# Kernel optimization log

Measured on AMD Instinct MI355X. Metric: run time of the kernel, lower is better.

## Reference

```python
import jax, jax.numpy as jnp
import numpy as np

HEADS = 4
EPS_LN = 1e-6
EPS_IN = 1e-5


def _ln(x, g, b):
    m = x.mean(-1, keepdims=True)
    v = ((x - m) ** 2).mean(-1, keepdims=True)
    return (x - m) / jnp.sqrt(v + EPS_LN) * g + b


def _inorm(s):
    # nn.InstanceNorm2d(1) (affine=False): normalize each (batch, channel=head)
    # slice over the last two (N, N) dims, biased variance, eps=1e-5.
    m = s.mean((-2, -1), keepdims=True)
    v = ((s - m) ** 2).mean((-2, -1), keepdims=True)
    return (s - m) / jnp.sqrt(v + EPS_IN)


def setup_inputs() -> dict:
    key = jax.random.key(0)
    ks = jax.random.split(key, 32)
    B, C, Hh = 8, 256, HEADS
    sc = 1.0 / np.sqrt(C)

    def n(k, shape, s):
        return jax.random.normal(k, shape, jnp.float32) * s

    return {
        "x": n(ks[0], (B, C, 6, 6, 6), 1.0),
        # global branch params
        "g_tok_w": n(ks[1], (C,), 0.05), "g_tok_b": jnp.zeros((C,), jnp.float32),
        "g_ln1_g": jnp.ones((C,), jnp.float32), "g_ln1_b": jnp.zeros((C,), jnp.float32),
        "g_wq": n(ks[2], (C, C * Hh), sc), "g_wk": n(ks[3], (C, C * Hh), sc),
        "g_wv": n(ks[4], (C, C * Hh), sc), "g_wo": n(ks[5], (C * Hh, C), sc),
        "g_ln2_g": jnp.ones((C,), jnp.float32), "g_ln2_b": jnp.zeros((C,), jnp.float32),
        "g_mo_w": n(ks[6], (C, C), sc), "g_mo_b": jnp.zeros((C,), jnp.float32),
        # local branch params
        "l_pw": n(ks[7], (8, 8), 0.35), "l_pb": jnp.zeros((8,), jnp.float32),
        "l_ln1_g": jnp.ones((C,), jnp.float32), "l_ln1_b": jnp.zeros((C,), jnp.float32),
        "l_wq": n(ks[8], (C, C * Hh), sc), "l_wk": n(ks[9], (C, C * Hh), sc),
        "l_wv": n(ks[10], (C, C * Hh), sc), "l_wo": n(ks[11], (C * Hh, C), sc),
        "l_ln2_g": jnp.ones((C,), jnp.float32), "l_ln2_b": jnp.zeros((C,), jnp.float32),
        "l_mo_w": n(ks[12], (C, C), sc), "l_mo_b": jnp.zeros((C,), jnp.float32),
    }


def _global_branch(x, tok_w, tok_b, ln1_g, ln1_b, wq, wk, wv, wo, ln2_g, ln2_b, mo_w, mo_b):
    B, C, D, H, W = x.shape
    Hh = HEADS
    # TokenLearner_Global: conv1x1x1 (1->256) then mean over (D,H,W), then
    # view(B,C,C).mean(dim=1).  Since the conv is 1x1 on a single input channel,
    # this collapses exactly to: w * mean(x over C,D,H,W) + b.
    m = x.mean((1, 2, 3, 4))                       # (B,)
    tok = m[:, None] * tok_w + tok_b               # (B, C)
    res = tok
    t = _ln(tok, ln1_g, ln1_b)                     # (B, C)
    q = (t @ wq).reshape(B, Hh, C)                 # heads outer in the 1024 split
    k = (t @ wk).reshape(B, Hh, C)
    v = (t @ wv).reshape(B, Hh, C)
    # mh_q^T (B,h,C,1) @ mh_k (B,h,1,C) -> rank-1 (B,h,C,C) score map
    score = q[:, :, :, None] * k[:, :, None, :]
    a = jax.nn.softmax(_inorm(score), axis=-1)
    o = jnp.einsum('bhij,bhj->bhi', a, v)          # attn @ mh_v^T -> (B,h,C)
    # permute(0,3,2,1).view: flatten as (c, heads) with c outer
    o = o.transpose(0, 2, 1).reshape(B, C * Hh)
    out = o @ wo                                   # (B, C)
    tok2 = _ln(out + res, ln2_g, ln2_b)            # (B, C)
    # map_out conv1x1 + GELU on a spatially-constant expand -> compute once
    g = jax.nn.gelu(jnp.einsum('bc,oc->bo', tok2, mo_w) + mo_b, approximate=False)
    return jnp.broadcast_to(g[:, :, None, None, None], (B, C, D, H, W))


def _local_branch(x, pw, pb, ln1_g, ln1_b, wq, wk, wv, wo, ln2_g, ln2_b, mo_w, mo_b):
    B, C, D, H, W = x.shape
    Hh = HEADS
    # TokenLearner_Local: conv3d(1->8, k=2, s=2) per channel == patchify 2x2x2
    xp = x.reshape(B * C, 3, 2, 3, 2, 3, 2).transpose(0, 1, 3, 5, 2, 4, 6)
    xp = xp.reshape(B * C, 27, 8)                  # (BC, patches, patch_vol)
    tok = xp @ pw.T + pb                           # (BC, 27, 8) embed_dim=8
    tok = tok.reshape(B, C, 3, 3, 3, 2, 2, 2)
    # res: (b c)(d h w)(p1 p2 p3) -> b (d p1 h p2 w p3) c
    res = tok.transpose(0, 2, 5, 3, 6, 4, 7, 1).reshape(B, 216, C)
    # attn input: (b c)(d h w)(p1 p2 p3) -> (b d h w) (p1 p2 p3) c
    e = tok.reshape(B, C, 3, 3, 3, 8).transpose(0, 2, 3, 4, 5, 1).reshape(B * 27, 8, C)
    e = _ln(e, ln1_g, ln1_b)
    # (c heads) split: c outer, heads inner
    q = (e @ wq).reshape(B * 27, 8, C, Hh).transpose(0, 3, 2, 1)   # (B27,h,C,8)
    k = (e @ wk).reshape(B * 27, 8, C, Hh).transpose(0, 3, 1, 2)   # (B27,h,8,C)
    v = (e @ wv).reshape(B * 27, 8, C, Hh).transpose(0, 3, 2, 1)   # (B27,h,C,8)
    score = q @ k                                                  # (B27,h,C,C)
    a = jax.nn.softmax(_inorm(score), axis=-1)
    o = a @ v                                                      # (B27,h,C,8)
    # (b d h w) heads c (p1 p2 p3) -> b (d p1 h p2 w p3) (c heads)
    o = o.reshape(B, 3, 3, 3, Hh, C, 2, 2, 2)
    o = o.transpose(0, 1, 6, 2, 7, 3, 8, 5, 4).reshape(B, 216, C * Hh)
    out = o @ wo                                                   # (B,216,C)
    t2 = _ln(out + res, ln2_g, ln2_b)
    xm = t2.transpose(0, 2, 1).reshape(B, C, D, H, W)
    return jax.nn.gelu(
        jnp.einsum('bcdhw,oc->bodhw', xm, mo_w) + mo_b[None, :, None, None, None],
        approximate=False)


def reference(x,
              g_tok_w, g_tok_b, g_ln1_g, g_ln1_b, g_wq, g_wk, g_wv, g_wo,
              g_ln2_g, g_ln2_b, g_mo_w, g_mo_b,
              l_pw, l_pb, l_ln1_g, l_ln1_b, l_wq, l_wk, l_wv, l_wo,
              l_ln2_g, l_ln2_b, l_mo_w, l_mo_b):
    g = _global_branch(x, g_tok_w, g_tok_b, g_ln1_g, g_ln1_b, g_wq, g_wk, g_wv,
                       g_wo, g_ln2_g, g_ln2_b, g_mo_w, g_mo_b)
    l = _local_branch(x, l_pw, l_pb, l_ln1_g, l_ln1_b, l_wq, l_wk, l_wv,
                      l_wo, l_ln2_g, l_ln2_b, l_mo_w, l_mo_b)
    return x + g + l
```

## Files before the change

kernel.cpp:

```cpp
#include <hip/hip_runtime.h>
#include <stdint.h>
#include <math.h>

#define DEVFN __device__ __forceinline__
typedef unsigned short u16;
typedef short bf16x8 __attribute__((ext_vector_type(8)));
typedef float f32x4  __attribute__((ext_vector_type(4)));

DEVFN float blk_sum(float v, float* s4) {
  #pragma unroll
  for (int o = 32; o > 0; o >>= 1) v += __shfl_down(v, o, 64);
  __syncthreads();
  if ((threadIdx.x & 63) == 0) s4[threadIdx.x >> 6] = v;
  __syncthreads();
  return s4[0] + s4[1] + s4[2] + s4[3];
}

DEVFN float gelu_f(float x) {
  return 0.5f * x * (1.f + erff(x * 0.7071067811865475f));
}

DEVFN u16 bf16_rne(float f) {
  uint32_t u = __float_as_uint(f);
  return (u16)((u + 0x7fffu + ((u >> 16) & 1u)) >> 16);
}

DEVFN float bf2f(u16 v) { return __uint_as_float(((uint32_t)v) << 16); }

DEVFN void gload16(const u16* g, u16* l) {
  auto gp = (const __attribute__((address_space(1))) uint32_t*)(uintptr_t)g;
  auto lp = (__attribute__((address_space(3))) uint32_t*)(uintptr_t)l;
  __builtin_amdgcn_global_load_lds(gp, lp, 16, 0, 0);
}

DEVFN void stage64x256(const u16* G, size_t gstride, u16* L, int w, int lane) {
  #pragma unroll
  for (int i = 0; i < 8; ++i) {
    int row = w * 16 + 2 * i + (lane >> 5);
    int c16 = (lane & 31) ^ (row & 7);
    gload16(G + (size_t)row * gstride + c16 * 8, L + (w * 16 + 2 * i) * 256);
  }
}

DEVFN bf16x8 lread(const u16* L, int row, int k16) {
  return *(const bf16x8*)&L[row * 256 + ((k16 ^ (row & 7)) << 3)];
}

DEVFN void trc_tile(const float* __restrict__ in, u16* __restrict__ out,
                    int R, int C, int r0, int c0, float (*tile)[33], int tid) {
  int tx = tid & 31, ty = tid >> 5;
  for (int i = ty; i < 32; i += 8) tile[i][tx] = in[(size_t)(r0 + i) * C + c0 + tx];
  __syncthreads();
  for (int i = ty; i < 32; i += 8)
    out[(size_t)(c0 + i) * R + r0 + tx] = bf16_rne(tile[tx][i]);
}

__global__ __launch_bounds__(256) void k_l_tok_prep(
    const float* __restrict__ x, const float* __restrict__ pw,
    const float* __restrict__ pb, const float* __restrict__ g1,
    const float* __restrict__ b1, float* __restrict__ res,
    u16* __restrict__ eln_bf, float* __restrict__ g_part,
    const float* __restrict__ wq, const float* __restrict__ wk,
    const float* __restrict__ wv, const float* __restrict__ wo,
    const float* __restrict__ mow, u16* __restrict__ WcatT,
    u16* __restrict__ woT, u16* __restrict__ moB) {
  __shared__ __align__(16) char smem[8448];
  int bid0 = blockIdx.x, tid = threadIdx.x;
  if (bid0 < 1728) {
    float* pws = (float*)smem;
    float* s4 = (float*)(smem + 256);
    int t = bid0;
    int b = t / 216, s = t % 216;
    int z = s / 36, y = (s / 6) % 6, xx = s % 6;
    int d = z >> 1, p1 = z & 1, hh = y >> 1, p2 = y & 1, ww = xx >> 1, p3 = xx & 1;
    int p = p1 * 4 + p2 * 2 + p3;
    int c = tid;
    if (c < 64) pws[c] = pw[c];
    __syncthreads();
    const float* xb = x + (b * 256 + c) * 216 + (2 * d) * 36 + (2 * hh) * 6 + 2 * ww;
    float v = pb[p];
    float xs = 0.f;
    #pragma unroll
    for (int q1 = 0; q1 < 2; ++q1)
      #pragma unroll
      for (int q2 = 0; q2 < 2; ++q2)
        #pragma unroll
        for (int q3 = 0; q3 < 2; ++q3) {
          float xv = xb[q1 * 36 + q2 * 6 + q3];
          xs += xv;
          v += xv * pws[p * 8 + (q1 * 4 + q2 * 2 + q3)];
        }
    float bs = blk_sum(xs, s4);
    if (c == 0) g_part[t] = bs;
    res[t * 256 + c] = v;
    float mu = blk_sum(v, s4) * (1.f / 256.f);
    float dd = v - mu;
    float var = blk_sum(dd * dd, s4) * (1.f / 256.f);
    eln_bf[t * 256 + c] = bf16_rne(dd * rsqrtf(var + 1e-6f) * g1[c] + b1[c]);
  } else {
    float (*tile)[33] = (float(*)[33])smem;
    int bid = bid0 - 1728;
    if (bid < 768) {
      int which = bid >> 8, b2 = bid & 255;
      const float* in = (which == 0) ? wq : (which == 1) ? wk : wv;
      u16* out = WcatT + which * 262144;
      int r0 = (b2 & 7) * 32, c0 = (b2 >> 3) * 32;
      trc_tile(in, out, 256, 1024, r0, c0, tile, tid);
    } else if (bid < 1024) {
      int b2 = bid - 768;
      int r0 = (b2 & 31) * 32, c0 = (b2 >> 5) * 32;
      trc_tile(wo, woT, 1024, 256, r0, c0, tile, tid);
    } else {
      int i = (bid - 1024) * 256 + tid;
      moB[i] = bf16_rne(mow[i]);
    }
  }
}

__global__ __launch_bounds__(256) void k_gemm_qkv_fused(
    const u16* __restrict__ A, const u16* __restrict__ BT, u16* __restrict__ C,
    const float* __restrict__ g_part, const float* __restrict__ tw_,
    const float* __restrict__ tb_, const float* __restrict__ g1,
    const float* __restrict__ b1, const float* __restrict__ wq,
    const float* __restrict__ wk, const float* __restrict__ wv,
    float* __restrict__ gqkv) {
  __shared__ __align__(16) char smem[65536];
  int bid = blockIdx.x, tid = threadIdx.x;
  if (bid < 1296) {
    const int N = 3072, K = 256;
    u16* aL = (u16*)smem;
    u16* bL = (u16*)smem + 16384;
    int rowblk = (bid % 27) * 64, colblk = (bid / 27) * 64;
    int lane = tid & 63, w = tid >> 6;
    int wr = (w >> 1) * 32, wc = (w & 1) * 32;
    int fm = lane & 15, lg = lane >> 4;
    stage64x256(A + (size_t)rowblk * K, K, aL, w, lane);
    stage64x256(BT + (size_t)colblk * K, K, bL, w, lane);
    __syncthreads();
    f32x4 acc[2][2] = {};
    #pragma unroll
    for (int kk = 0; kk < 8; ++kk) {
      int k16 = kk * 4 + lg;
      bf16x8 bn0 = lread(bL, wc + fm, k16);
      bf16x8 bn1 = lread(bL, wc + 16 + fm, k16);
      bf16x8 af0 = lread(aL, wr + fm, k16);
      bf16x8 af1 = lread(aL, wr + 16 + fm, k16);
      acc[0][0] = __builtin_amdgcn_mfma_f32_16x16x32_bf16(af0, bn0, acc[0][0], 0, 0, 0);
      acc[0][1] = __builtin_amdgcn_mfma_f32_16x16x32_bf16(af0, bn1, acc[0][1], 0, 0, 0);
      acc[1][0] = __builtin_amdgcn_mfma_f32_16x16x32_bf16(af1, bn0, acc[1][0], 0, 0, 0);
      acc[1][1] = __builtin_amdgcn_mfma_f32_16x16x32_bf16(af1, bn1, acc[1][1], 0, 0, 0);
    }
    __syncthreads();
    u16* ct = (u16*)smem;
    #pragma unroll
    for (int mi = 0; mi < 2; ++mi)
      #pragma unroll
      for (int ni = 0; ni < 2; ++ni)
        #pragma unroll
        for (int r = 0; r < 4; ++r)
          ct[(wr + mi * 16 + lg * 4 + r) * 64 + wc + ni * 16 + fm] = bf16_rne(acc[mi][ni][r]);
    __syncthreads();
    #pragma unroll
    for (int pass = 0; pass < 2; ++pass) {
      int id = pass * 256 + tid;
      int r = id >> 3, u = id & 7;
      *(uint4*)&C[(size_t)(rowblk + r) * N + colblk + u * 8] = *(uint4*)&ct[r * 64 + u * 8];
    }
  } else {
    float* ts = (float*)smem;
    float (*red)[4][8] = (float(*)[4][8])(smem + 8192);
    float* s4 = (float*)(smem + 16384);
    float* m_s = (float*)(smem + 16400);
    int rb = bid - 1296;
    float tw = tw_[tid], tb = tb_[tid], gg = g1[tid], bb = b1[tid];
    float S1 = blk_sum(tw, s4);
    float S2 = blk_sum(tw * tw, s4);
    float S3 = blk_sum(tb, s4);
    float S4 = blk_sum(tb * tb, s4);
    float S5 = blk_sum(tw * tb, s4);
    {
      int b = tid >> 5, sl = tid & 31;
      float a = 0.f;
      for (int k = sl; k < 216; k += 32) a += g_part[b * 216 + k];
      #pragma unroll
      for (int o = 16; o > 0; o >>= 1) a += __shfl_down(a, o, 32);
      if (sl == 0) m_s[b] = a * (1.f / 442368.f);
    }
    __syncthreads();
    #pragma unroll
    for (int b = 0; b < 8; ++b) {
      float m = m_s[b];
      float mu = (m * S1 + S3) * (1.f / 256.f);
      float var = (m * m * S2 + 2.f * m * S5 + S4) * (1.f / 256.f) - mu * mu;
      ts[b * 256 + tid] = (m * tw + tb - mu) * rsqrtf(var + 1e-6f) * gg + bb;
    }
    __syncthreads();
    int col0 = rb * 64;
    int cl = tid & 63, kq = tid >> 6;
    int col = col0 + cl;
    int m = col >> 10, cc = col & 1023;
    const float* W = (m == 0) ? wq : (m == 1) ? wk : wv;
    float acc[8] = {};
    for (int c = kq * 64; c < kq * 64 + 64; ++c) {
      float w = W[c * 1024 + cc];
      #pragma unroll
      for (int b = 0; b < 8; ++b) acc[b] = fmaf(ts[b * 256 + c], w, acc[b]);
    }
    #pragma unroll
    for (int b = 0; b < 8; ++b) red[cl][kq][b] = acc[b];
    __syncthreads();
    if (kq == 0) {
      #pragma unroll
      for (int b = 0; b < 8; ++b)
        gqkv[b * 3072 + col] = red[cl][0][b] + red[cl][1][b] + red[cl][2][b] + red[cl][3][b];
    }
  }
}

__global__ __launch_bounds__(256) void k_l_attn_fused(
    const u16* __restrict__ qkv, u16* __restrict__ o_buf,
    const float* __restrict__ gq, float* __restrict__ g_o) {
  __shared__ __align__(16) uint4 Qb[256], Kb[256];
  __shared__ __align__(16) u16 vt[16][264];
  __shared__ __align__(16) u16 Pl[256][72];
  __shared__ float rqA[64][4], rkA[64][4], rlq[64][4], rlk[64][4], s_ab[2];
  int bid = blockIdx.x, tid = threadIdx.x;
  if (bid >= 864) {
    float* ks = (float*)Qb;
    float* vs = ks + 256;
    float* s4 = (float*)Kb;
    int idx = bid - 864;
    int b = idx >> 2, h = idx & 3;
    int i = tid;
    const float* base = gq + b * 3072 + h * 256;
    float q = base[i];
    float k = base[1024 + i];
    ks[i] = k;
    vs[i] = base[2048 + i];
    float sq  = blk_sum(q, s4);
    float sq2 = blk_sum(q * q, s4);
    float sk  = blk_sum(k, s4);
    float sk2 = blk_sum(k * k, s4);
    float tot  = sq * sk * (1.f / 65536.f);
    float tot2 = sq2 * sk2 * (1.f / 65536.f);
    float rstd = rsqrtf(tot2 - tot * tot + 1e-5f);
    float A = rstd, B = -tot * rstd;
    float den = 0.f, num = 0.f;
    for (int j = 0; j < 256; ++j) {
      float w = __expf(fmaf(q * ks[j], A, B));
      den += w; num += w * vs[j];
    }
    g_o[b * 1024 + (i << 2) + h] = num / den;
    return;
  }
  int n = bid >> 2, h = bid & 3;
  int b = n / 27, patch = n % 27;
  int bz = 2 * (patch / 9), by = 2 * ((patch / 3) % 3), bx = 2 * (patch % 3);
  int tid2 = tid;
  {
    int c = tid2;
    u16 qv[8], kv[8], vv[8];
    #pragma unroll
    for (int p = 0; p < 8; ++p) {
      int t_l = b * 216 + (bz + (p >> 2)) * 36 + (by + ((p >> 1) & 1)) * 6 + (bx + (p & 1));
      const u16* row = qkv + (size_t)t_l * 3072 + (c << 2) + h;
      qv[p] = row[0]; kv[p] = row[1024]; vv[p] = row[2048];
    }
    uint32_t qw[4], kw[4];
    #pragma unroll
    for (int i = 0; i < 4; ++i) {
      qw[i] = (uint32_t)qv[2 * i] | ((uint32_t)qv[2 * i + 1] << 16);
      kw[i] = (uint32_t)kv[2 * i] | ((uint32_t)kv[2 * i + 1] << 16);
    }
    Qb[c] = make_uint4(qw[0], qw[1], qw[2], qw[3]);
    Kb[c] = make_uint4(kw[0], kw[1], kw[2], kw[3]);
    #pragma unroll
    for (int p = 0; p < 8; ++p) vt[p][c] = vv[p];
    vt[8][c] = 0x3F80u;
    #pragma unroll
    for (int r2 = 9; r2 < 16; ++r2) vt[r2][c] = 0;
  }
  __syncthreads();
  {
    int p = tid2 & 63, chunk = tid2 >> 6;
    int d = p >> 3, e = p & 7;
    float aq = 0.f, ak = 0.f, lq = 0.f, lk = 0.f;
    for (int cc = chunk * 64; cc < chunk * 64 + 64; ++cc) {
      const u16* qr = (const u16*)&Qb[cc];
      const u16* kr = (const u16*)&Kb[cc];
      float qd = bf2f(qr[d]), qe = bf2f(qr[e]);
      float kd = bf2f(kr[d]), ke = bf2f(kr[e]);
      aq = fmaf(qd, qe, aq); ak = fmaf(kd, ke, ak);
      if (e == 0) { lq += qd; lk += kd; }
    }
    rqA[p][chunk] = aq; rkA[p][chunk] = ak; rlq[p][chunk] = lq; rlk[p][chunk] = lk;
    __syncthreads();
    if (tid2 < 64) {
      float gq2 = rqA[tid2][0] + rqA[tid2][1] + rqA[tid2][2] + rqA[tid2][3];
      float gk = rkA[tid2][0] + rkA[tid2][1] + rkA[tid2][2] + rkA[tid2][3];
      float vprod = gq2 * gk, vmu = 0.f;
      if ((tid2 & 7) == 0) {
        float slq = rlq[tid2][0] + rlq[tid2][1] + rlq[tid2][2] + rlq[tid2][3];
        float slk = rlk[tid2][0] + rlk[tid2][1] + rlk[tid2][2] + rlk[tid2][3];
        vmu = slq * slk;
      }
      #pragma unroll
      for (int o = 32; o > 0; o >>= 1) {
        vprod += __shfl_down(vprod, o, 64);
        vmu   += __shfl_down(vmu, o, 64);
      }
      if (tid2 == 0) {
        float mu = vmu * (1.f / 65536.f), m2 = vprod * (1.f / 65536.f);
        float rstd = rsqrtf(m2 - mu * mu + 1e-5f);
        s_ab[0] = rstd; s_ab[1] = -mu * rstd;
      }
    }
    __syncthreads();
  }
  float Af = s_ab[0], Bf = s_ab[1];
  int lane = tid2 & 63, w = tid2 >> 6;
  int l15 = lane & 15, lg = lane >> 4;
  bf16x8 qf[4];
  #pragma unroll
  for (int qt = 0; qt < 4; ++qt)
    qf[qt] = *(const bf16x8*)&Qb[w * 64 + qt * 16 + l15];
  f32x4 acc_o[4] = {};
  #pragma unroll 1
  for (int jc = 0; jc < 4; ++jc) {
    bf16x8 kf[4];
    #pragma unroll
    for (int jt = 0; jt < 4; ++jt) {
      bf16x8 z = {};
      if (lg == 0) z = *(const bf16x8*)&Kb[jc * 64 + jt * 16 + l15];
      kf[jt] = z;
    }
    #pragma unroll
    for (int jt = 0; jt < 4; ++jt) {
      #pragma unroll
      for (int qt = 0; qt < 4; ++qt) {
        f32x4 zc = {};
        f32x4 s = __builtin_amdgcn_mfma_f32_16x16x32_bf16(kf[jt], qf[qt], zc, 0, 0, 0);
        float e0 = __expf(fmaf(s[0], Af, Bf));
        float e1 = __expf(fmaf(s[1], Af, Bf));
        float e2 = __expf(fmaf(s[2], Af, Bf));
        float e3 = __expf(fmaf(s[3], Af, Bf));
        uint32_t w0 = (__float_as_uint(e0) >> 16) | (__float_as_uint(e1) & 0xFFFF0000u);
        uint32_t w1 = (__float_as_uint(e2) >> 16) | (__float_as_uint(e3) & 0xFFFF0000u);
        int q = w * 64 + qt * 16 + l15;
        *(uint2*)&Pl[q][jt * 16 + lg * 4] = make_uint2(w0, w1);
      }
    }
    #pragma unroll
    for (int ks2 = 0; ks2 < 2; ++ks2) {
      bf16x8 vf = *(const bf16x8*)&vt[l15][jc * 64 + ks2 * 32 + lg * 8];
      #pragma unroll
      for (int qt = 0; qt < 4; ++qt) {
        bf16x8 pf = *(const bf16x8*)&Pl[w * 64 + qt * 16 + l15][ks2 * 32 + lg * 8];
        acc_o[qt] = __builtin_amdgcn_mfma_f32_16x16x32_bf16(pf, vf, acc_o[qt], 0, 0, 0);
      }
    }
  }
  int src = ((lane & 48) + 8) << 2;
  int p = l15;
  int t_l = b * 216 + (bz + (p >> 2)) * 36 + (by + ((p >> 1) & 1)) * 6 + (bx + (p & 1));
  #pragma unroll
  for (int qt = 0; qt < 4; ++qt) {
    #pragma unroll
    for (int r = 0; r < 4; ++r) {
      float den = __int_as_float(__builtin_amdgcn_ds_bpermute(src, __float_as_int(acc_o[qt][r])));
      if (p < 8) {
        int q = w * 64 + qt * 16 + lg * 4 + r;
        o_buf[(size_t)t_l * 1024 + (q << 2) + h] = bf16_rne(acc_o[qt][r] / den);
      }
    }
  }
}

__global__ __launch_bounds__(256) void k_gemm_sk_fused(
    const u16* __restrict__ A, const u16* __restrict__ BT, float* __restrict__ Cp,
    const float* __restrict__ g_o, const float* __restrict__ wo,
    float* __restrict__ part) {
  __shared__ __align__(16) char smem[65536];
  int bid = blockIdx.x, tid = threadIdx.x;
  if (bid < 216) {
    const int M = 1728, N = 256, K = 1024;
    u16* aL = (u16*)smem;
    u16* bL = (u16*)smem + 16384;
    int rowblk = (bid % 27) * 64, colblk = ((bid / 27) & 3) * 64;
    int kz = bid / 108;
    float* C = Cp + (size_t)kz * M * N;
    int lane = tid & 63, w = tid >> 6;
    int wr = (w >> 1) * 32, wc = (w & 1) * 32;
    int fm = lane & 15, lg = lane >> 4;
    f32x4 acc[2][2] = {};
    #pragma unroll 1
    for (int step = 0; step < 2; ++step) {
      int kt = kz * 512 + step * 256;
      __syncthreads();
      stage64x256(A + (size_t)rowblk * K + kt, K, aL, w, lane);
      stage64x256(BT + (size_t)colblk * K + kt, K, bL, w, lane);
      __syncthreads();
      #pragma unroll
      for (int kk = 0; kk < 8; ++kk) {
        int k16 = kk * 4 + lg;
        bf16x8 bn0 = lread(bL, wc + fm, k16);
        bf16x8 bn1 = lread(bL, wc + 16 + fm, k16);
        bf16x8 af0 = lread(aL, wr + fm, k16);
        bf16x8 af1 = lread(aL, wr + 16 + fm, k16);
        acc[0][0] = __builtin_amdgcn_mfma_f32_16x16x32_bf16(af0, bn0, acc[0][0], 0, 0, 0);
        acc[0][1] = __builtin_amdgcn_mfma_f32_16x16x32_bf16(af0, bn1, acc[0][1], 0, 0, 0);
        acc[1][0] = __builtin_amdgcn_mfma_f32_16x16x32_bf16(af1, bn0, acc[1][0], 0, 0, 0);
        acc[1][1] = __builtin_amdgcn_mfma_f32_16x16x32_bf16(af1, bn1, acc[1][1], 0, 0, 0);
      }
    }
    __syncthreads();
    float* ct = (float*)smem;
    #pragma unroll
    for (int mi = 0; mi < 2; ++mi)
      #pragma unroll
      for (int ni = 0; ni < 2; ++ni)
        #pragma unroll
        for (int r = 0; r < 4; ++r)
          ct[(wr + mi * 16 + lg * 4 + r) * 64 + wc + ni * 16 + fm] = acc[mi][ni][r];
    __syncthreads();
    #pragma unroll
    for (int pass = 0; pass < 4; ++pass) {
      int id = pass * 256 + tid;
      int r = id >> 4, u = id & 15;
      *(float4*)&C[(size_t)(rowblk + r) * N + colblk + u * 4] = *(float4*)&ct[r * 64 + u * 4];
    }
  } else {
    float* os = (float*)smem;
    int kc = bid - 216;
    os[tid] = g_o[(tid >> 5) * 1024 + kc * 32 + (tid & 31)];
    __syncthreads();
    float acc[8] = {};
    #pragma unroll
    for (int kk = 0; kk < 32; ++kk) {
      float w = wo[(size_t)(kc * 32 + kk) * 256 + tid];
      #pragma unroll
      for (int b = 0; b < 8; ++b) acc[b] = fmaf(os[b * 32 + kk], w, acc[b]);
    }
    #pragma unroll
    for (int b = 0; b < 8; ++b) part[kc * 2048 + b * 256 + tid] = acc[b];
  }
}

__global__ __launch_bounds__(256) void k_l_ln2_fused(
    const float* __restrict__ proj0, const float* __restrict__ proj1,
    const float* __restrict__ res, const float* __restrict__ g2,
    const float* __restrict__ b2, u16* __restrict__ t2b,
    const float* __restrict__ part, const float* __restrict__ g_part,
    const float* __restrict__ tw_, const float* __restrict__ tb_,
    const float* __restrict__ gg2, const float* __restrict__ gb2,
    float* __restrict__ t2g) {
  __shared__ float s4[4];
  int bid = blockIdx.x, c = threadIdx.x;
  if (bid < 1728) {
    int t = bid;
    float v = proj0[t * 256 + c] + proj1[t * 256 + c] + res[t * 256 + c];
    float mu = blk_sum(v, s4) * (1.f / 256.f);
    float d = v - mu;
    float var = blk_sum(d * d, s4) * (1.f / 256.f);
    t2b[t * 256 + c] = bf16_rne(d * rsqrtf(var + 1e-6f) * g2[c] + b2[c]);
  } else {
    int b = bid - 1728;
    float a = (c < 216) ? g_part[b * 216 + c] : 0.f;
    float m = blk_sum(a, s4) * (1.f / 442368.f);
    float v = m * tw_[c] + tb_[c];
    #pragma unroll
    for (int kc = 0; kc < 32; ++kc) v += part[kc * 2048 + b * 256 + c];
    float mu = blk_sum(v, s4) * (1.f / 256.f);
    float d = v - mu;
    float var = blk_sum(d * d, s4) * (1.f / 256.f);
    t2g[b * 256 + c] = d * rsqrtf(var + 1e-6f) * gg2[c] + gb2[c];
  }
}

__global__ __launch_bounds__(256) void k_g_mo(
    const float* __restrict__ t2g, const float* __restrict__ mow,
    const float* __restrict__ mob, float* __restrict__ g_vec) {
  __shared__ float ts[2048];
  int tid = threadIdx.x;
  for (int i = tid; i < 2048; i += 256) ts[i] = t2g[i];
  __syncthreads();
  int ol = tid >> 5, cs = tid & 31;
  int o = blockIdx.x * 8 + ol;
  const float* wrow = mow + (size_t)o * 256;
  float acc[8] = {};
  #pragma unroll
  for (int i = 0; i < 8; ++i) {
    float w = wrow[i * 32 + cs];
    #pragma unroll
    for (int b = 0; b < 8; ++b) acc[b] = fmaf(ts[b * 256 + i * 32 + cs], w, acc[b]);
  }
  #pragma unroll
  for (int b = 0; b < 8; ++b) {
    float v = acc[b];
    #pragma unroll
    for (int off = 16; off > 0; off >>= 1) v += __shfl_down(v, off, 32);
    if (cs == 0) g_vec[b * 256 + o] = gelu_f(v + mob[o]);
  }
}

__global__ __launch_bounds__(256) void k_gemm_mo_final(
    const u16* __restrict__ A, const u16* __restrict__ BT,
    const float* __restrict__ x, const float* __restrict__ gvec,
    const float* __restrict__ mob, float* __restrict__ out) {
  __shared__ __align__(16) char smem[65536];
  u16* aL = (u16*)smem;
  u16* bL = (u16*)smem + 16384;
  float (*ct)[65] = (float(*)[65])smem;
  const int K = 256;
  int tid = threadIdx.x;
  int rowblk = blockIdx.x * 64, colblk = blockIdx.y * 64;
  int lane = tid & 63, w = tid >> 6;
  int wr = (w >> 1) * 32, wc = (w & 1) * 32;
  int fm = lane & 15, lg = lane >> 4;
  stage64x256(A + (size_t)rowblk * K, K, aL, w, lane);
  stage64x256(BT + (size_t)colblk * K, K, bL, w, lane);
  __syncthreads();
  f32x4 acc[2][2] = {};
  #pragma unroll
  for (int kk = 0; kk < 8; ++kk) {
    int k16 = kk * 4 + lg;
    bf16x8 bn0 = lread(bL, wc + fm, k16);
    bf16x8 bn1 = lread(bL, wc + 16 + fm, k16);
    bf16x8 af0 = lread(aL, wr + fm, k16);
    bf16x8 af1 = lread(aL, wr + 16 + fm, k16);
    acc[0][0] = __builtin_amdgcn_mfma_f32_16x16x32_bf16(af0, bn0, acc[0][0], 0, 0, 0);
    acc[0][1] = __builtin_amdgcn_mfma_f32_16x16x32_bf16(af0, bn1, acc[0][1], 0, 0, 0);
    acc[1][0] = __builtin_amdgcn_mfma_f32_16x16x32_bf16(af1, bn0, acc[1][0], 0, 0, 0);
    acc[1][1] = __builtin_amdgcn_mfma_f32_16x16x32_bf16(af1, bn1, acc[1][1], 0, 0, 0);
  }
  __syncthreads();
  int row_l0 = wr + lg * 4;
  #pragma unroll
  for (int mi = 0; mi < 2; ++mi)
    #pragma unroll
    for (int ni = 0; ni < 2; ++ni)
      #pragma unroll
      for (int r = 0; r < 4; ++r)
        ct[row_l0 + mi * 16 + r][wc + ni * 16 + fm] = acc[mi][ni][r];
  __syncthreads();
  int s_l = tid & 63;
  #pragma unroll 4
  for (int pass = 0; pass < 16; ++pass) {
    int col_l = (tid >> 6) * 16 + pass;
    int row = rowblk + s_l, col = colblk + col_l;
    int b = row / 216, s = row - b * 216;
    size_t idx = (size_t)b * 55296 + (size_t)col * 216 + s;
    out[idx] = x[idx] + gvec[b * 256 + col] + gelu_f(ct[s_l][col_l] + mob[col]);
  }
}

extern "C" void kernel_launch(void* const* d_in, const int* in_sizes, int n_in,
                              void* d_out, int out_size, void* d_ws, size_t ws_size,
                              hipStream_t stream) {
  const float* x     = (const float*)d_in[0];
  const float* g_tw  = (const float*)d_in[1];
  const float* g_tb  = (const float*)d_in[2];
  const float* g_l1g = (const float*)d_in[3];
  const float* g_l1b = (const float*)d_in[4];
  const float* g_wq  = (const float*)d_in[5];
  const float* g_wk  = (const float*)d_in[6];
  const float* g_wv  = (const float*)d_in[7];
  const float* g_wo  = (const float*)d_in[8];
  const float* g_l2g = (const float*)d_in[9];
  const float* g_l2b = (const float*)d_in[10];
  const float* g_mow = (const float*)d_in[11];
  const float* g_mob = (const float*)d_in[12];
  const float* l_pw  = (const float*)d_in[13];
  const float* l_pb  = (const float*)d_in[14];
  const float* l_l1g = (const float*)d_in[15];
  const float* l_l1b = (const float*)d_in[16];
  const float* l_wq  = (const float*)d_in[17];
  const float* l_wk  = (const float*)d_in[18];
  const float* l_wv  = (const float*)d_in[19];
  const float* l_wo  = (const float*)d_in[20];
  const float* l_l2g = (const float*)d_in[21];
  const float* l_l2b = (const float*)d_in[22];
  const float* l_mow = (const float*)d_in[23];
  const float* l_mob = (const float*)d_in[24];
  float* out = (float*)d_out;
  float* ws  = (float*)d_ws;

  float* g_qkv  = ws + 4096;
  float* g_o    = ws + 28672;
  float* g_vec  = ws + 36864;
  float* g_part = ws + 38912;
  float* res    = ws + 40960;
  u16*   eln_bf = (u16*)(ws + 483328);
  u16*   WcatT  = (u16*)(ws + 704512);
  u16*   woT    = (u16*)(ws + 1097728);
  u16*   moB    = (u16*)(ws + 1228800);
  u16*   qkvb   = (u16*)(ws + 1261568);
  u16*   o_buf  = (u16*)(ws + 6569984);
  float* proj   = ws + 7454720;
  u16*   t2b    = (u16*)(ws + 8339456);
  float* part_wo= ws + 8560640;
  float* t2g    = ws + 8626176;

  k_l_tok_prep<<<3008, 256, 0, stream>>>(x, l_pw, l_pb, l_l1g, l_l1b,
                                         res, eln_bf, g_part,
                                         l_wq, l_wk, l_wv, l_wo, l_mow,
                                         WcatT, woT, moB);
  k_gemm_qkv_fused<<<1344, 256, 0, stream>>>(eln_bf, WcatT, qkvb,
                                             g_part, g_tw, g_tb, g_l1g, g_l1b,
                                             g_wq, g_wk, g_wv, g_qkv);
  k_l_attn_fused<<<896, 256, 0, stream>>>(qkvb, o_buf, g_qkv, g_o);
  k_gemm_sk_fused<<<248, 256, 0, stream>>>(o_buf, woT, proj, g_o, g_wo, part_wo);
  k_l_ln2_fused<<<1736, 256, 0, stream>>>(proj, proj + 442368, res,
                                          l_l2g, l_l2b, t2b,
                                          part_wo, g_part, g_tw, g_tb,
                                          g_l2g, g_l2b, t2g);
  k_g_mo<<<32, 256, 0, stream>>>(t2g, g_mow, g_mob, g_vec);
  k_gemm_mo_final<<<dim3(27, 4), 256, 0, stream>>>(t2b, moB, x, g_vec, l_mob, out);
}
```

Baseline: 99.78 us.

## Split QKV GEMM from global branch, remap tiles, fuse LayerNorm reductions

Moves the global-branch QKV projection out of the fused GEMM launch into its own small kernel, so the local GEMM no longer reserves 64 KB of generic shared memory. The GEMM now stages tiles in a k-major LDS layout without XOR swizzle, remaps block indices to group tiles, and pads the output staging stride to 72. LayerNorm statistics are computed with single-pass sum and sum-of-squares reductions, which cuts the number of block barriers. The single-pass variance is less numerically robust, and the extra launch adds a serial kernel boundary.

```diff
diff --git a/kernel.cpp b/kernel.cpp
--- a/kernel.cpp
+++ b/kernel.cpp
@@ -16,6 +16,40 @@
   return s4[0] + s4[1] + s4[2] + s4[3];
 }
 
+DEVFN void blk_sum3(float a, float b, float c, float* out, float (*s)[4]) {
+  #pragma unroll
+  for (int o = 32; o > 0; o >>= 1) {
+    a += __shfl_down(a, o, 64);
+    b += __shfl_down(b, o, 64);
+    c += __shfl_down(c, o, 64);
+  }
+  __syncthreads();
+  if ((threadIdx.x & 63) == 0) {
+    int wi = threadIdx.x >> 6;
+    s[0][wi] = a; s[1][wi] = b; s[2][wi] = c;
+  }
+  __syncthreads();
+  out[0] = s[0][0] + s[0][1] + s[0][2] + s[0][3];
+  out[1] = s[1][0] + s[1][1] + s[1][2] + s[1][3];
+  out[2] = s[2][0] + s[2][1] + s[2][2] + s[2][3];
+}
+
+DEVFN void blk_sum2(float a, float b, float* out, float (*s)[4]) {
+  #pragma unroll
+  for (int o = 32; o > 0; o >>= 1) {
+    a += __shfl_down(a, o, 64);
+    b += __shfl_down(b, o, 64);
+  }
+  __syncthreads();
+  if ((threadIdx.x & 63) == 0) {
+    int wi = threadIdx.x >> 6;
+    s[0][wi] = a; s[1][wi] = b;
+  }
+  __syncthreads();
+  out[0] = s[0][0] + s[0][1] + s[0][2] + s[0][3];
+  out[1] = s[1][0] + s[1][1] + s[1][2] + s[1][3];
+}
+
 DEVFN float gelu_f(float x) {
   return 0.5f * x * (1.f + erff(x * 0.7071067811865475f));
 }
@@ -41,7 +75,6 @@
     gload16(G + (size_t)row * gstride + c16 * 8, L + (w * 16 + 2 * i) * 256);
   }
 }
-
 DEVFN bf16x8 lread(const u16* L, int row, int k16) {
   return *(const bf16x8*)&L[row * 256 + ((k16 ^ (row & 7)) << 3)];
 }
@@ -68,7 +101,7 @@
   int bid0 = blockIdx.x, tid = threadIdx.x;
   if (bid0 < 1728) {
     float* pws = (float*)smem;
-    float* s4 = (float*)(smem + 256);
+    float (*s3)[4] = (float(*)[4])(smem + 256);
     int t = bid0;
     int b = t / 216, s = t % 216;
     int z = s / 36, y = (s / 6) % 6, xx = s % 6;
@@ -90,13 +123,13 @@
           xs += xv;
           v += xv * pws[p * 8 + (q1 * 4 + q2 * 2 + q3)];
         }
-    float bs = blk_sum(xs, s4);
-    if (c == 0) g_part[t] = bs;
+    float r3[3];
+    blk_sum3(xs, v, v * v, r3, s3);
+    if (c == 0) g_part[t] = r3[0];
     res[t * 256 + c] = v;
-    float mu = blk_sum(v, s4) * (1.f / 256.f);
-    float dd = v - mu;
-    float var = blk_sum(dd * dd, s4) * (1.f / 256.f);
-    eln_bf[t * 256 + c] = bf16_rne(dd * rsqrtf(var + 1e-6f) * g1[c] + b1[c]);
+    float mu = r3[1] * (1.f / 256.f);
+    float var = r3[2] * (1.f / 256.f) - mu * mu;
+    eln_bf[t * 256 + c] = bf16_rne((v - mu) * rsqrtf(var + 1e-6f) * g1[c] + b1[c]);
   } else {
     float (*tile)[33] = (float(*)[33])smem;
     int bid = bid0 - 1728;
@@ -117,103 +150,106 @@
   }
 }
 
-__global__ __launch_bounds__(256) void k_gemm_qkv_fused(
-    const u16* __restrict__ A, const u16* __restrict__ BT, u16* __restrict__ C,
+__global__ __launch_bounds__(256) void k_gemm_qkv(
+    const u16* __restrict__ A, const u16* __restrict__ BT, u16* __restrict__ C) {
+  __shared__ __align__(16) u16 aL[16384];
+  __shared__ __align__(16) u16 bL[16384];
+  const int N = 3072, K = 256;
+  int bid = blockIdx.x;
+  int tile = (bid & 7) * 162 + (bid >> 3);
+  int rowblk = (tile % 27) * 64, colblk = (tile / 27) * 64;
+  int tid = threadIdx.x, lane = tid & 63, w = tid >> 6;
+  int wr = (w >> 1) * 32, wc = (w & 1) * 32;
+  int fm = lane & 15, lg = lane >> 4;
+  #pragma unroll
+  for (int i = 0; i < 8; ++i) {
+    int c16 = w * 8 + i;
+    gload16(&A[(size_t)(rowblk + lane) * K + c16 * 8], aL + c16 * 512);
+    gload16(&BT[(size_t)(colblk + lane) * K + c16 * 8], bL + c16 * 512);
+  }
+  __syncthreads();
+  f32x4 acc[2][2] = {};
+  #pragma unroll
+  for (int kk = 0; kk < 8; ++kk) {
+    int k16 = kk * 4 + lg;
+    bf16x8 bn0 = *(const bf16x8*)&bL[k16 * 512 + (wc + fm) * 8];
+    bf16x8 bn1 = *(const bf16x8*)&bL[k16 * 512 + (wc + 16 + fm) * 8];
+    bf16x8 af0 = *(const bf16x8*)&aL[k16 * 512 + (wr + fm) * 8];
+    bf16x8 af1 = *(const bf16x8*)&aL[k16 * 512 + (wr + 16 + fm) * 8];
+    acc[0][0] = __builtin_amdgcn_mfma_f32_16x16x32_bf16(af0, bn0, acc[0][0], 0, 0, 0);
+    acc[0][1] = __builtin_amdgcn_mfma_f32_16x16x32_bf16(af0, bn1, acc[0][1], 0, 0, 0);
+    acc[1][0] = __builtin_amdgcn_mfma_f32_16x16x32_bf16(af1, bn0, acc[1][0], 0, 0, 0);
+    acc[1][1] = __builtin_amdgcn_mfma_f32_16x16x32_bf16(af1, bn1, acc[1][1], 0, 0, 0);
+  }
+  __syncthreads();
+  u16* ct = aL;
+  #pragma unroll
+  for (int mi = 0; mi < 2; ++mi)
+    #pragma unroll
+    for (int ni = 0; ni < 2; ++ni)
+      #pragma unroll
+      for (int r = 0; r < 4; ++r)
+        ct[(wr + mi * 16 + lg * 4 + r) * 72 + wc + ni * 16 + fm] = bf16_rne(acc[mi][ni][r]);
+  __syncthreads();
+  #pragma unroll
+  for (int pass = 0; pass < 2; ++pass) {
+    int id = pass * 256 + tid;
+    int r = id >> 3, u = id & 7;
+    *(uint4*)&C[(size_t)(rowblk + r) * N + colblk + u * 8] = *(uint4*)&ct[r * 72 + u * 8];
+  }
+}
+
+__global__ __launch_bounds__(256) void k_g_qkv(
     const float* __restrict__ g_part, const float* __restrict__ tw_,
     const float* __restrict__ tb_, const float* __restrict__ g1,
     const float* __restrict__ b1, const float* __restrict__ wq,
     const float* __restrict__ wk, const float* __restrict__ wv,
     float* __restrict__ gqkv) {
-  __shared__ __align__(16) char smem[65536];
-  int bid = blockIdx.x, tid = threadIdx.x;
-  if (bid < 1296) {
-    const int N = 3072, K = 256;
-    u16* aL = (u16*)smem;
-    u16* bL = (u16*)smem + 16384;
-    int rowblk = (bid % 27) * 64, colblk = (bid / 27) * 64;
-    int lane = tid & 63, w = tid >> 6;
-    int wr = (w >> 1) * 32, wc = (w & 1) * 32;
-    int fm = lane & 15, lg = lane >> 4;
-    stage64x256(A + (size_t)rowblk * K, K, aL, w, lane);
-    stage64x256(BT + (size_t)colblk * K, K, bL, w, lane);
-    __syncthreads();
-    f32x4 acc[2][2] = {};
-    #pragma unroll
-    for (int kk = 0; kk < 8; ++kk) {
-      int k16 = kk * 4 + lg;
-      bf16x8 bn0 = lread(bL, wc + fm, k16);
-      bf16x8 bn1 = lread(bL, wc + 16 + fm, k16);
-      bf16x8 af0 = lread(aL, wr + fm, k16);
-      bf16x8 af1 = lread(aL, wr + 16 + fm, k16);
-      acc[0][0] = __builtin_amdgcn_mfma_f32_16x16x32_bf16(af0, bn0, acc[0][0], 0, 0, 0);
-      acc[0][1] = __builtin_amdgcn_mfma_f32_16x16x32_bf16(af0, bn1, acc[0][1], 0, 0, 0);
-      acc[1][0] = __builtin_amdgcn_mfma_f32_16x16x32_bf16(af1, bn0, acc[1][0], 0, 0, 0);
-      acc[1][1] = __builtin_amdgcn_mfma_f32_16x16x32_bf16(af1, bn1, acc[1][1], 0, 0, 0);
-    }
-    __syncthreads();
-    u16* ct = (u16*)smem;
-    #pragma unroll
-    for (int mi = 0; mi < 2; ++mi)
-      #pragma unroll
-      for (int ni = 0; ni < 2; ++ni)
-        #pragma unroll
-        for (int r = 0; r < 4; ++r)
-          ct[(wr + mi * 16 + lg * 4 + r) * 64 + wc + ni * 16 + fm] = bf16_rne(acc[mi][ni][r]);
-    __syncthreads();
-    #pragma unroll
-    for (int pass = 0; pass < 2; ++pass) {
-      int id = pass * 256 + tid;
-      int r = id >> 3, u = id & 7;
-      *(uint4*)&C[(size_t)(rowblk + r) * N + colblk + u * 8] = *(uint4*)&ct[r * 64 + u * 8];
-    }
-  } else {
-    float* ts = (float*)smem;
-    float (*red)[4][8] = (float(*)[4][8])(smem + 8192);
-    float* s4 = (float*)(smem + 16384);
-    float* m_s = (float*)(smem + 16400);
-    int rb = bid - 1296;
-    float tw = tw_[tid], tb = tb_[tid], gg = g1[tid], bb = b1[tid];
-    float S1 = blk_sum(tw, s4);
-    float S2 = blk_sum(tw * tw, s4);
-    float S3 = blk_sum(tb, s4);
-    float S4 = blk_sum(tb * tb, s4);
-    float S5 = blk_sum(tw * tb, s4);
-    {
-      int b = tid >> 5, sl = tid & 31;
-      float a = 0.f;
-      for (int k = sl; k < 216; k += 32) a += g_part[b * 216 + k];
-      #pragma unroll
-      for (int o = 16; o > 0; o >>= 1) a += __shfl_down(a, o, 32);
-      if (sl == 0) m_s[b] = a * (1.f / 442368.f);
-    }
-    __syncthreads();
-    #pragma unroll
-    for (int b = 0; b < 8; ++b) {
-      float m = m_s[b];
-      float mu = (m * S1 + S3) * (1.f / 256.f);
-      float var = (m * m * S2 + 2.f * m * S5 + S4) * (1.f / 256.f) - mu * mu;
-      ts[b * 256 + tid] = (m * tw + tb - mu) * rsqrtf(var + 1e-6f) * gg + bb;
-    }
-    __syncthreads();
-    int col0 = rb * 64;
-    int cl = tid & 63, kq = tid >> 6;
-    int col = col0 + cl;
-    int m = col >> 10, cc = col & 1023;
-    const float* W = (m == 0) ? wq : (m == 1) ? wk : wv;
-    float acc[8] = {};
-    for (int c = kq * 64; c < kq * 64 + 64; ++c) {
-      float w = W[c * 1024 + cc];
-      #pragma unroll
-      for (int b = 0; b < 8; ++b) acc[b] = fmaf(ts[b * 256 + c], w, acc[b]);
-    }
-    #pragma unroll
-    for (int b = 0; b < 8; ++b) red[cl][kq][b] = acc[b];
-    __syncthreads();
-    if (kq == 0) {
-      #pragma unroll
-      for (int b = 0; b < 8; ++b)
-        gqkv[b * 3072 + col] = red[cl][0][b] + red[cl][1][b] + red[cl][2][b] + red[cl][3][b];
-    }
+  __shared__ float ts[2048];
+  __shared__ float red[64][4][8];
+  __shared__ float s4[4], m_s[8];
+  int tid = threadIdx.x;
+  float tw = tw_[tid], tb = tb_[tid], gg = g1[tid], bb = b1[tid];
+  float S1 = blk_sum(tw, s4);
+  float S2 = blk_sum(tw * tw, s4);
+  float S3 = blk_sum(tb, s4);
+  float S4 = blk_sum(tb * tb, s4);
+  float S5 = blk_sum(tw * tb, s4);
+  {
+    int b = tid >> 5, sl = tid & 31;
+    float a = 0.f;
+    for (int k = sl; k < 216; k += 32) a += g_part[b * 216 + k];
+    #pragma unroll
+    for (int o = 16; o > 0; o >>= 1) a += __shfl_down(a, o, 32);
+    if (sl == 0) m_s[b] = a * (1.f / 442368.f);
+  }
+  __syncthreads();
+  #pragma unroll
+  for (int b = 0; b < 8; ++b) {
+    float m = m_s[b];
+    float mu = (m * S1 + S3) * (1.f / 256.f);
+    float var = (m * m * S2 + 2.f * m * S5 + S4) * (1.f / 256.f) - mu * mu;
+    ts[b * 256 + tid] = (m * tw + tb - mu) * rsqrtf(var + 1e-6f) * gg + bb;
+  }
+  __syncthreads();
+  int col0 = blockIdx.x * 64;
+  int cl = tid & 63, kq = tid >> 6;
+  int col = col0 + cl;
+  int m = col >> 10, cc = col & 1023;
+  const float* W = (m == 0) ? wq : (m == 1) ? wk : wv;
+  float acc[8] = {};
+  for (int c = kq * 64; c < kq * 64 + 64; ++c) {
+    float w = W[c * 1024 + cc];
+    #pragma unroll
+    for (int b = 0; b < 8; ++b) acc[b] = fmaf(ts[b * 256 + c], w, acc[b]);
+  }
+  #pragma unroll
+  for (int b = 0; b < 8; ++b) red[cl][kq][b] = acc[b];
+  __syncthreads();
+  if (kq == 0) {
+    #pragma unroll
+    for (int b = 0; b < 8; ++b)
+      gqkv[b * 3072 + col] = red[cl][0][b] + red[cl][1][b] + red[cl][2][b] + red[cl][3][b];
   }
 }
 
@@ -256,9 +292,8 @@
   int n = bid >> 2, h = bid & 3;
   int b = n / 27, patch = n % 27;
   int bz = 2 * (patch / 9), by = 2 * ((patch / 3) % 3), bx = 2 * (patch % 3);
-  int tid2 = tid;
   {
-    int c = tid2;
+    int c = tid;
     u16 qv[8], kv[8], vv[8];
     #pragma unroll
     for (int p = 0; p < 8; ++p) {
@@ -282,7 +317,7 @@
   }
   __syncthreads();
   {
-    int p = tid2 & 63, chunk = tid2 >> 6;
+    int p = tid & 63, chunk = tid >> 6;
     int d = p >> 3, e = p & 7;
     float aq = 0.f, ak = 0.f, lq = 0.f, lk = 0.f;
     for (int cc = chunk * 64; cc < chunk * 64 + 64; ++cc) {
@@ -295,13 +330,13 @@
     }
     rqA[p][chunk] = aq; rkA[p][chunk] = ak; rlq[p][chunk] = lq; rlk[p][chunk] = lk;
     __syncthreads();
-    if (tid2 < 64) {
-      float gq2 = rqA[tid2][0] + rqA[tid2][1] + rqA[tid2][2] + rqA[tid2][3];
-      float gk = rkA[tid2][0] + rkA[tid2][1] + rkA[tid2][2] + rkA[tid2][3];
+    if (tid < 64) {
+      float gq2 = rqA[tid][0] + rqA[tid][1] + rqA[tid][2] + rqA[tid][3];
+      float gk = rkA[tid][0] + rkA[tid][1] + rkA[tid][2] + rkA[tid][3];
       float vprod = gq2 * gk, vmu = 0.f;
-      if ((tid2 & 7) == 0) {
-        float slq = rlq[tid2][0] + rlq[tid2][1] + rlq[tid2][2] + rlq[tid2][3];
-        float slk = rlk[tid2][0] + rlk[tid2][1] + rlk[tid2][2] + rlk[tid2][3];
+      if ((tid & 7) == 0) {
+        float slq = rlq[tid][0] + rlq[tid][1] + rlq[tid][2] + rlq[tid][3];
+        float slk = rlk[tid][0] + rlk[tid][1] + rlk[tid][2] + rlk[tid][3];
         vmu = slq * slk;
       }
       #pragma unroll
@@ -309,7 +344,7 @@
         vprod += __shfl_down(vprod, o, 64);
         vmu   += __shfl_down(vmu, o, 64);
       }
-      if (tid2 == 0) {
+      if (tid == 0) {
         float mu = vmu * (1.f / 65536.f), m2 = vprod * (1.f / 65536.f);
         float rstd = rsqrtf(m2 - mu * mu + 1e-5f);
         s_ab[0] = rstd; s_ab[1] = -mu * rstd;
@@ -318,7 +353,7 @@
     __syncthreads();
   }
   float Af = s_ab[0], Bf = s_ab[1];
-  int lane = tid2 & 63, w = tid2 >> 6;
+  int lane = tid & 63, w = tid >> 6;
   int l15 = lane & 15, lg = lane >> 4;
   bf16x8 qf[4];
   #pragma unroll
@@ -454,26 +489,28 @@
     const float* __restrict__ tw_, const float* __restrict__ tb_,
     const float* __restrict__ gg2, const float* __restrict__ gb2,
     float* __restrict__ t2g) {
-  __shared__ float s4[4];
+  __shared__ float s2v[2][4];
   int bid = blockIdx.x, c = threadIdx.x;
   if (bid < 1728) {
     int t = bid;
     float v = proj0[t * 256 + c] + proj1[t * 256 + c] + res[t * 256 + c];
-    float mu = blk_sum(v, s4) * (1.f / 256.f);
-    float d = v - mu;
-    float var = blk_sum(d * d, s4) * (1.f / 256.f);
-    t2b[t * 256 + c] = bf16_rne(d * rsqrtf(var + 1e-6f) * g2[c] + b2[c]);
+    float r2[2];
+    blk_sum2(v, v * v, r2, s2v);
+    float mu = r2[0] * (1.f / 256.f);
+    float var = r2[1] * (1.f / 256.f) - mu * mu;
+    t2b[t * 256 + c] = bf16_rne((v - mu) * rsqrtf(var + 1e-6f) * g2[c] + b2[c]);
   } else {
     int b = bid - 1728;
     float a = (c < 216) ? g_part[b * 216 + c] : 0.f;
-    float m = blk_sum(a, s4) * (1.f / 442368.f);
+    float m = blk_sum(a, (float*)s2v) * (1.f / 442368.f);
     float v = m * tw_[c] + tb_[c];
     #pragma unroll
     for (int kc = 0; kc < 32; ++kc) v += part[kc * 2048 + b * 256 + c];
-    float mu = blk_sum(v, s4) * (1.f / 256.f);
-    float d = v - mu;
-    float var = blk_sum(d * d, s4) * (1.f / 256.f);
-    t2g[b * 256 + c] = d * rsqrtf(var + 1e-6f) * gg2[c] + gb2[c];
+    float r2[2];
+    blk_sum2(v, v * v, r2, s2v);
+    float mu = r2[0] * (1.f / 256.f);
+    float var = r2[1] * (1.f / 256.f) - mu * mu;
+    t2g[b * 256 + c] = (v - mu) * rsqrtf(var + 1e-6f) * gg2[c] + gb2[c];
   }
 }
 
@@ -605,9 +642,9 @@
                                          res, eln_bf, g_part,
                                          l_wq, l_wk, l_wv, l_wo, l_mow,
                                          WcatT, woT, moB);
-  k_gemm_qkv_fused<<<1344, 256, 0, stream>>>(eln_bf, WcatT, qkvb,
-                                             g_part, g_tw, g_tb, g_l1g, g_l1b,
-                                             g_wq, g_wk, g_wv, g_qkv);
+  k_gemm_qkv<<<1296, 256, 0, stream>>>(eln_bf, WcatT, qkvb);
+  k_g_qkv<<<48, 256, 0, stream>>>(g_part, g_tw, g_tb, g_l1g, g_l1b,
+                                  g_wq, g_wk, g_wv, g_qkv);
   k_l_attn_fused<<<896, 256, 0, stream>>>(qkvb, o_buf, g_qkv, g_o);
   k_gemm_sk_fused<<<248, 256, 0, stream>>>(o_buf, woT, proj, g_o, g_wo, part_wo);
   k_l_ln2_fused<<<1736, 256, 0, stream>>>(proj, proj + 442368, res,
```

Measured after the change: 117.2 us. 17.4% more time.
